# Kernel optimization log

Measured on AMD Instinct MI355X. Metric: run time of the kernel, lower is better.

Reference implementation:

```python
import jax, jax.numpy as jnp
import numpy as np

NH = 16      # num_attention_heads
NKV = 8      # num_key_value_heads
G = NH // NKV  # num_key_value_groups
D = 128      # head_dim = hidden_size // NH
ROPE_MAX = 2048


def _rope_tables(seq_len, dtype=jnp.float32):
    # matches RotaryEmbedding: inv_freq over even dims, freqs duplicated (concat), cos/sin cached
    inv_freq = 1.0 / (10000.0 ** (jnp.arange(0, D, 2, dtype=jnp.float32) / D))
    t = jnp.arange(ROPE_MAX, dtype=jnp.float32)[:, None]          # [max, 1]
    freqs = t * inv_freq[None, :]                                  # [max, D/2]
    freqs = jnp.concatenate((freqs, freqs), axis=-1)               # [max, D]
    cos = jnp.cos(freqs)[:seq_len].astype(dtype)                   # [S, D]
    sin = jnp.sin(freqs)[:seq_len].astype(dtype)
    # unsqueeze(0) then unsqueeze(2) -> [1, S, 1, D] broadcasting over batch and heads
    return cos[None, :, None, :], sin[None, :, None, :]


def _rotate_half(x):
    x1, x2 = jnp.split(x, 2, axis=-1)
    return jnp.concatenate((-x2, x1), axis=-1)


def setup_inputs() -> dict:
    key = jax.random.key(0)
    ks = jax.random.split(key, 5)
    B, S, H = 2, 2048, 2048
    scale = 1.0 / np.sqrt(H)
    return {
        "hidden_states": jax.random.normal(ks[0], (B, S, H), jnp.float32),
        "Wq": jax.random.normal(ks[1], (H, H), jnp.float32) * scale,
        "Wk": jax.random.normal(ks[2], (NKV * D, H), jnp.float32) * scale,
        "Wv": jax.random.normal(ks[3], (NKV * D, H), jnp.float32) * scale,
        "Wo": jax.random.normal(ks[4], (H, H), jnp.float32) * scale,
    }


def reference(hidden_states, Wq, Wk, Wv, Wo):
    B, S, H = hidden_states.shape
    # projections (nn.Linear: y = x @ W.T, no bias)
    q = (hidden_states @ Wq.T).reshape(B, S, NH, D)     # [B,S,NH,D]
    k = (hidden_states @ Wk.T).reshape(B, S, NKV, D)    # [B,S,NKV,D]
    v = (hidden_states @ Wv.T).reshape(B, S, NKV, D)

    cos, sin = _rope_tables(S, hidden_states.dtype)
    q = q * cos + _rotate_half(q) * sin
    k = k * cos + _rotate_half(k) * sin

    # GQA: query head h attends to kv head h // G (repeat_kv ordering: h = n*G + g)
    qg = q.reshape(B, S, NKV, G, D).transpose(0, 2, 3, 1, 4)   # [B,NKV,G,S,D]
    kt = k.transpose(0, 2, 1, 3)                                # [B,NKV,S,D]
    vt = v.transpose(0, 2, 1, 3)                                # [B,NKV,S,D]

    scores = jnp.einsum("bngqd,bnkd->bngqk", qg, kt) / np.sqrt(D)  # [B,NKV,G,S,S]
    causal = jnp.triu(jnp.ones((S, S), dtype=bool), k=1)
    neg = jnp.finfo(scores.dtype).min
    scores = jnp.where(causal[None, None, None], neg, scores)
    probs = jax.nn.softmax(scores.astype(jnp.float32), axis=-1).astype(q.dtype)

    out = jnp.einsum("bngqk,bnkd->bngqd", probs, vt)            # [B,NKV,G,S,D]
    out = out.transpose(0, 3, 1, 2, 4).reshape(B, S, H)         # [B,S,H]
    return out @ Wo.T
```

## Files before the change

kernel.cpp:

```cpp
#include <hip/hip_runtime.h>

typedef unsigned short u16;
typedef __attribute__((ext_vector_type(8))) short short8;
typedef __attribute__((ext_vector_type(4))) float f32x4;

__device__ __forceinline__ u16 f2bf(float f) {
  unsigned u = __float_as_uint(f);
  return (u16)((u + 0x7FFFu + ((u >> 16) & 1u)) >> 16);
}
__device__ __forceinline__ float bf2f(u16 h) {
  return __uint_as_float(((unsigned)h) << 16);
}

__device__ __forceinline__ void gload_lds16(const void* g, void* l) {
  __builtin_amdgcn_global_load_lds(
      (const __attribute__((address_space(1))) unsigned*)g,
      (__attribute__((address_space(3))) unsigned*)l, 16, 0, 0);
}

__global__ void cast_f32_bf16_k(const float4* __restrict__ in, u16* __restrict__ out, int n4) {
  int i = blockIdx.x * 256 + threadIdx.x;
  if (i >= n4) return;
  float4 v = in[i];
  union { u16 u[4]; uint2 d; } r;
  r.u[0] = f2bf(v.x); r.u[1] = f2bf(v.y); r.u[2] = f2bf(v.z); r.u[3] = f2bf(v.w);
  *reinterpret_cast<uint2*>(out + (size_t)i * 4) = r.d;
}

__global__ void rope_tables_k(float* __restrict__ cosT, float* __restrict__ sinT) {
  int idx = blockIdx.x * 256 + threadIdx.x;
  int i = idx & 63, s = idx >> 6;
  double inv = pow(10000.0, -(double)(2 * i) / 128.0);
  double f = (double)s * inv;
  cosT[idx] = (float)cos(f);
  sinT[idx] = (float)sin(f);
}

__global__ void rope_q_k(u16* __restrict__ x, const float* __restrict__ cosT,
                         const float* __restrict__ sinT) {
  int idx = blockIdx.x * 256 + threadIdx.x;
  int i = idx & 63;
  int hh = (idx >> 6) & 15;
  int row = idx >> 10;
  int s = row & 2047;
  size_t base = (size_t)row * 4096 + hh * 128;
  float x1 = bf2f(x[base + i]);
  float x2 = bf2f(x[base + i + 64]);
  float c = cosT[s * 64 + i], sn = sinT[s * 64 + i];
  x[base + i]      = f2bf(x1 * c - x2 * sn);
  x[base + i + 64] = f2bf(x2 * c + x1 * sn);
}

__global__ void rope_repack_k_k(const u16* __restrict__ qkv, u16* __restrict__ kt,
                                const float* __restrict__ cosT, const float* __restrict__ sinT) {
  int idx = blockIdx.x * 256 + threadIdx.x;
  int i = idx & 63;
  int kvh = (idx >> 6) & 7;
  int row = idx >> 9;
  int s = row & 2047, b = row >> 11;
  size_t src = (size_t)row * 4096 + 2048 + kvh * 128;
  float x1 = bf2f(qkv[src + i]);
  float x2 = bf2f(qkv[src + i + 64]);
  float c = cosT[s * 64 + i], sn = sinT[s * 64 + i];
  size_t dst = ((size_t)(b * 8 + kvh) * 2048 + s) * 128;
  kt[dst + i]      = f2bf(x1 * c - x2 * sn);
  kt[dst + i + 64] = f2bf(x2 * c + x1 * sn);
}

__global__ void transpose_v_k(const u16* __restrict__ qkv, u16* __restrict__ vt) {
  __shared__ u16 tile[128][129];
  int bn = blockIdx.y;
  int s0 = blockIdx.x * 128;
  int b = bn >> 3, n = bn & 7;
  for (int e = threadIdx.x; e < 128 * 128; e += 256) {
    int r = e >> 7, c = e & 127;
    tile[r][c] = qkv[(size_t)(b * 2048 + s0 + r) * 4096 + 3072 + n * 128 + c];
  }
  __syncthreads();
  for (int e = threadIdx.x; e < 128 * 128; e += 256) {
    int r = e >> 7, c = e & 127;
    vt[((size_t)bn * 128 + r) * 2048 + s0 + c] = tile[c][r];
  }
}

template<typename OutT, int BN>
__global__ __launch_bounds__(512, 1) void gemm256_k(
    const u16* __restrict__ A, const u16* __restrict__ Bm,
    OutT* __restrict__ C, int M, int N, int K)
{
  constexpr int BITER = (BN * 8) / 512;
  constexpr int NFR = BN / 64;
  __shared__ __align__(16) u16 As[2][256 * 64];
  __shared__ __align__(16) u16 Bs[2][BN * 64];
  const int tid = threadIdx.x;
  const int wave = tid >> 6, lane = tid & 63;
  const int wm = wave >> 2, wn = wave & 3;
  const int lrow = lane & 15, lgrp = lane >> 4;
  const int gx = (int)gridDim.x;
  const int nwg = gx * (int)gridDim.y;
  const int f = (int)(blockIdx.y * gridDim.x + blockIdx.x);
  const int sw = (f & 7) * (nwg >> 3) + (f >> 3);
  const int bx = sw % gx, by = sw / gx;
  const int row0 = by * 256, col0 = bx * BN;

  f32x4 acc[8][NFR];
  #pragma unroll
  for (int m = 0; m < 8; ++m)
    #pragma unroll
    for (int n = 0; n < NFR; ++n) acc[m][n] = (f32x4){0.f, 0.f, 0.f, 0.f};

  const int NT = K >> 6;

  auto stage = [&](int buf, int k0) {
    #pragma unroll
    for (int i = 0; i < 4; ++i) {
      int cid = i * 512 + tid;
      int row = cid >> 3, cp = cid & 7;
      int c = cp ^ (row & 7);
      gload_lds16(A + (size_t)(row0 + row) * K + k0 + c * 8,
                  &As[buf][(size_t)(i * 512 + wave * 64) * 8]);
    }
    #pragma unroll
    for (int i = 0; i < BITER; ++i) {
      int cid = i * 512 + tid;
      int row = cid >> 3, cp = cid & 7;
      int c = cp ^ (row & 7);
      gload_lds16(Bm + (size_t)(col0 + row) * K + k0 + c * 8,
                  &Bs[buf][(size_t)(i * 512 + wave * 64) * 8]);
    }
  };

  stage(0, 0);
  for (int t = 0; t < NT; ++t) {
    const int cur = t & 1;
    if (t + 1 < NT) {
      stage(cur ^ 1, (t + 1) << 6);
      if constexpr (BN == 256) asm volatile("s_waitcnt vmcnt(8)" ::: "memory");
      else                     asm volatile("s_waitcnt vmcnt(6)" ::: "memory");
    } else {
      asm volatile("s_waitcnt vmcnt(0)" ::: "memory");
    }
    __builtin_amdgcn_s_barrier();
    __builtin_amdgcn_sched_barrier(0);
    #pragma unroll
    for (int ks = 0; ks < 2; ++ks) {
      short8 af[8], bfr[NFR];
      #pragma unroll
      for (int m = 0; m < 8; ++m) {
        int row = wm * 128 + m * 16 + lrow;
        int cp = (ks * 4 + lgrp) ^ (row & 7);
        af[m] = *reinterpret_cast<const short8*>(&As[cur][row * 64 + cp * 8]);
      }
      #pragma unroll
      for (int n = 0; n < NFR; ++n) {
        int row = wn * (NFR * 16) + n * 16 + lrow;
        int cp = (ks * 4 + lgrp) ^ (row & 7);
        bfr[n] = *reinterpret_cast<const short8*>(&Bs[cur][row * 64 + cp * 8]);
      }
      #pragma unroll
      for (int m = 0; m < 8; ++m)
        #pragma unroll
        for (int n = 0; n < NFR; ++n)
          acc[m][n] = __builtin_amdgcn_mfma_f32_16x16x32_bf16(af[m], bfr[n], acc[m][n], 0, 0, 0);
    }
    __builtin_amdgcn_sched_barrier(0);
    __builtin_amdgcn_s_barrier();
  }

  #pragma unroll
  for (int m = 0; m < 8; ++m)
    #pragma unroll
    for (int n = 0; n < NFR; ++n)
      #pragma unroll
      for (int j = 0; j < 4; ++j) {
        int r = row0 + wm * 128 + m * 16 + lgrp * 4 + j;
        int col = col0 + wn * (NFR * 16) + n * 16 + lrow;
        float val = acc[m][n][j];
        if constexpr (sizeof(OutT) == 2) C[(size_t)r * N + col] = f2bf(val);
        else                             C[(size_t)r * N + col] = val;
      }
}

__global__ __launch_bounds__(256, 2) void flash_attn_k(
    const u16* __restrict__ qkv, const u16* __restrict__ kt,
    const u16* __restrict__ vt, u16* __restrict__ o)
{
  constexpr int S = 2048, NH = 16, NKV = 8, D = 128;
  const int wave = threadIdx.x >> 6, lane = threadIdx.x & 63;
  const int flat = blockIdx.x;
  const int pr = flat >> 5;
  const int bh = (flat & 7) * 4 + ((flat >> 3) & 3);
  const int b = bh >> 4, h = bh & 15;
  const int kvh = h >> 1;
  const int lrow = lane & 15, lgrp = lane >> 4;

  __shared__ __align__(16) u16 ks[2][64 * 128];
  __shared__ __align__(16) u16 vs[2][128 * 64];

  const float scl2 = 0.12754245006443634f;
  const u16* khead = kt + (size_t)(b * NKV + kvh) * S * D;
  const u16* vhead = vt + (size_t)(b * NKV + kvh) * D * S;

  auto stage = [&](int nxt, int kv0n) {
    #pragma unroll
    for (int i = 0; i < 4; ++i) {
      int c = i * 256 + wave * 64 + lane;
      int kr = c >> 4;
      int kc16 = (c & 15) ^ (kr & 7);
      gload_lds16(khead + (size_t)(kv0n + kr) * D + kc16 * 8,
                  &ks[nxt][(size_t)(i * 256 + wave * 64) * 8]);
      int vr = c >> 3;
      int vc = (c & 7) ^ (vr & 7);
      gload_lds16(vhead + (size_t)vr * S + kv0n + vc * 8,
                  &vs[nxt][(size_t)(i * 256 + wave * 64) * 8]);
    }
  };

  #pragma unroll
  for (int ph = 0; ph < 2; ++ph) {
    const int qt = ph ? pr : (31 - pr);
    const int q0 = qt * 64 + wave * 16;
    const int trips = qt + 1;

    short8 qf[4];
    const u16* qbase = qkv + (size_t)(b * S + q0 + lrow) * 4096 + h * 128;
    #pragma unroll
    for (int kc = 0; kc < 4; ++kc)
      qf[kc] = *reinterpret_cast<const short8*>(qbase + kc * 32 + lgrp * 8);

    f32x4 acc[8];
    #pragma unroll
    for (int n = 0; n < 8; ++n) acc[n] = (f32x4){0.f, 0.f, 0.f, 0.f};
    float l_part[4] = {0.f, 0.f, 0.f, 0.f};

    stage(0, 0);
    __syncthreads();

    for (int t = 0; t < trips; ++t) {
      const int cur = t & 1;
      const int kv0 = t * 64;
      f32x4 sc[4];
      #pragma unroll
      for (int nb = 0; nb < 4; ++nb) {
        sc[nb] = (f32x4){0.f, 0.f, 0.f, 0.f};
        const int r = nb * 16 + lrow;
        #pragma unroll
        for (int kc = 0; kc < 4; ++kc) {
          int ch = (kc * 4 + lgrp) ^ (r & 7);
          short8 kf = *reinterpret_cast<const short8*>(&ks[cur][r * 128 + ch * 8]);
          sc[nb] = __builtin_amdgcn_mfma_f32_16x16x32_bf16(qf[kc], kf, sc[nb], 0, 0, 0);
        }
      }
      __syncthreads();
      if (t + 1 < trips) stage(cur ^ 1, kv0 + 64);
      u16* pb = &ks[cur][wave * 1024];
      if (t < trips - 1) {
        #pragma unroll
        for (int nb = 0; nb < 4; ++nb)
          #pragma unroll
          for (int j = 0; j < 4; ++j) {
            int qr = lgrp * 4 + j;
            float p = exp2f(fminf(sc[nb][j] * scl2, 43.f));
            l_part[j] += p;
            pb[qr * 64 + ((nb * 16 + lrow) ^ ((qr & 7) << 3))] = f2bf(p);
          }
      } else {
        #pragma unroll
        for (int nb = 0; nb < 4; ++nb) {
          if (nb < wave) {
            #pragma unroll
            for (int j = 0; j < 4; ++j) {
              int qr = lgrp * 4 + j;
              float p = exp2f(fminf(sc[nb][j] * scl2, 43.f));
              l_part[j] += p;
              pb[qr * 64 + ((nb * 16 + lrow) ^ ((qr & 7) << 3))] = f2bf(p);
            }
          } else if (nb == wave) {
            #pragma unroll
            for (int j = 0; j < 4; ++j) {
              int qr = lgrp * 4 + j;
              float p = (lrow <= qr) ? exp2f(fminf(sc[nb][j] * scl2, 43.f)) : 0.f;
              l_part[j] += p;
              pb[qr * 64 + ((nb * 16 + lrow) ^ ((qr & 7) << 3))] = f2bf(p);
            }
          } else {
            #pragma unroll
            for (int j = 0; j < 4; ++j) {
              int qr = lgrp * 4 + j;
              pb[qr * 64 + ((nb * 16 + lrow) ^ ((qr & 7) << 3))] = 0;
            }
          }
        }
      }
      short8 pf[2];
      #pragma unroll
      for (int kc2 = 0; kc2 < 2; ++kc2) {
        int ch = (kc2 * 4 + lgrp) ^ (lrow & 7);
        pf[kc2] = *reinterpret_cast<const short8*>(&pb[lrow * 64 + ch * 8]);
      }
      #pragma unroll
      for (int n = 0; n < 8; ++n) {
        const int d = n * 16 + lrow;
        #pragma unroll
        for (int kc2 = 0; kc2 < 2; ++kc2) {
          int ch = (kc2 * 4 + lgrp) ^ (d & 7);
          short8 vf = *reinterpret_cast<const short8*>(&vs[cur][d * 64 + ch * 8]);
          acc[n] = __builtin_amdgcn_mfma_f32_16x16x32_bf16(pf[kc2], vf, acc[n], 0, 0, 0);
        }
      }
      __syncthreads();
    }

    float inv[4];
    #pragma unroll
    for (int j = 0; j < 4; ++j) {
      float s = l_part[j];
      #pragma unroll
      for (int off = 8; off; off >>= 1) s += __shfl_xor(s, off);
      inv[j] = 1.f / s;
    }
    u16* obase = o + (((size_t)(b * S + q0)) * NH + h) * D;
    #pragma unroll
    for (int n = 0; n < 8; ++n)
      #pragma unroll
      for (int j = 0; j < 4; ++j)
        obase[(size_t)(lgrp * 4 + j) * NH * D + n * 16 + lrow] = f2bf(acc[n][j] * inv[j]);
    __syncthreads();
  }
}

extern "C" void kernel_launch(void* const* d_in, const int* in_sizes, int n_in,
                              void* d_out, int out_size, void* d_ws, size_t ws_size,
                              hipStream_t stream) {
  const float* hs = (const float*)d_in[0];
  const float* Wq = (const float*)d_in[1];
  const float* Wk = (const float*)d_in[2];
  const float* Wv = (const float*)d_in[3];
  const float* Wo = (const float*)d_in[4];
  float* out = (float*)d_out;

  constexpr int B = 2, S = 2048, H = 2048, NH = 16, NKV = 8, D = 128;
  constexpr int M = B * S;
  constexpr int NQKV = 4096;

  char* w = (char*)d_ws;
  auto alloc = [&](size_t bytes) { char* p = w; w += (bytes + 255) & ~(size_t)255; return p; };
  u16* hs_bf   = (u16*)alloc((size_t)M * H * 2);
  u16* wqkv_bf = (u16*)alloc((size_t)NQKV * H * 2);
  u16* wo_bf   = (u16*)alloc((size_t)H * H * 2);
  u16* qkv     = (u16*)alloc((size_t)M * NQKV * 2);
  float* cosT  = (float*)alloc((size_t)S * 64 * 4);
  float* sinT  = (float*)alloc((size_t)S * 64 * 4);
  u16* attn = hs_bf;
  u16* vt   = wqkv_bf;
  u16* kt   = wqkv_bf + (size_t)B * NKV * D * S;

  cast_f32_bf16_k<<<(M * H / 4) / 256, 256, 0, stream>>>((const float4*)hs, hs_bf, M * H / 4);
  cast_f32_bf16_k<<<(H * H / 4) / 256, 256, 0, stream>>>((const float4*)Wq, wqkv_bf, H * H / 4);
  cast_f32_bf16_k<<<(NKV * D * H / 4) / 256, 256, 0, stream>>>((const float4*)Wk, wqkv_bf + (size_t)2048 * H, NKV * D * H / 4);
  cast_f32_bf16_k<<<(NKV * D * H / 4) / 256, 256, 0, stream>>>((const float4*)Wv, wqkv_bf + (size_t)3072 * H, NKV * D * H / 4);
  cast_f32_bf16_k<<<(H * H / 4) / 256, 256, 0, stream>>>((const float4*)Wo, wo_bf, H * H / 4);
  rope_tables_k<<<(S * 64) / 256, 256, 0, stream>>>(cosT, sinT);

  gemm256_k<u16, 256><<<dim3(NQKV / 256, M / 256), 512, 0, stream>>>(hs_bf, wqkv_bf, qkv, M, NQKV, H);

  rope_q_k<<<(M * 16 * 64) / 256, 256, 0, stream>>>(qkv, cosT, sinT);
  rope_repack_k_k<<<(M * 8 * 64) / 256, 256, 0, stream>>>(qkv, kt, cosT, sinT);
  transpose_v_k<<<dim3(S / 128, B * NKV), 256, 0, stream>>>(qkv, vt);

  flash_attn_k<<<512, 256, 0, stream>>>(qkv, kt, vt, attn);

  gemm256_k<float, 128><<<dim3(H / 128, M / 256), 512, 0, stream>>>(attn, wo_bf, out, M, H, H);
}
```

Baseline: 238.0 us.

## Add finer-grained pipelined 256x256 GEMM for QKV projection

Adds a new GEMM kernel that splits each 64-wide K tile into two 32-wide halves and interleaves the prefetch of the next tile's A/B halves between MFMA groups. It uses explicit vmcnt waits, barriers and setprio so global-to-LDS loads overlap matrix-core work. The QKV projection now uses this kernel. The trade-offs are more barriers per K tile and a hand-tuned wait schedule that must stay correct.

```diff
diff --git a/kernel.cpp b/kernel.cpp
--- a/kernel.cpp
+++ b/kernel.cpp
@@ -81,6 +81,146 @@
     int r = e >> 7, c = e & 127;
     vt[((size_t)bn * 128 + r) * 2048 + s0 + c] = tile[c][r];
   }
+}
+
+template<typename OutT>
+__global__ __launch_bounds__(512, 1) void gemm256p_k(
+    const u16* __restrict__ A, const u16* __restrict__ Bm,
+    OutT* __restrict__ C, int M, int N, int K)
+{
+  __shared__ __align__(16) u16 As[2][2][256 * 32];
+  __shared__ __align__(16) u16 Bs[2][2][256 * 32];
+  const int tid = threadIdx.x;
+  const int wave = tid >> 6, lane = tid & 63;
+  const int wm = wave >> 2, wn = wave & 3;
+  const int lrow = lane & 15, lgrp = lane >> 4;
+  const int gx = (int)gridDim.x;
+  const int nwg = gx * (int)gridDim.y;
+  const int f = (int)(blockIdx.y * gridDim.x + blockIdx.x);
+  const int sw = (f & 7) * (nwg >> 3) + (f >> 3);
+  const int bx = sw % gx, by = sw / gx;
+  const int row0 = by * 256, col0 = bx * 256;
+
+  f32x4 acc[8][4];
+  #pragma unroll
+  for (int m = 0; m < 8; ++m)
+    #pragma unroll
+    for (int n = 0; n < 4; ++n) acc[m][n] = (f32x4){0.f, 0.f, 0.f, 0.f};
+
+  const int NT = K >> 6;
+  const int psw = lgrp ^ (lrow & 3);
+
+  auto stageA = [&](int buf, int t, int ks) {
+    const int k0 = (t << 6) + ks * 32;
+    #pragma unroll
+    for (int i = 0; i < 2; ++i) {
+      int s = i * 512 + tid;
+      int row = s >> 2, p = s & 3;
+      int g = p ^ (row & 3);
+      gload_lds16(A + (size_t)(row0 + row) * K + k0 + g * 8,
+                  &As[buf][ks][(size_t)(i * 512 + wave * 64) * 8]);
+    }
+  };
+  auto stageB = [&](int buf, int t, int ks) {
+    const int k0 = (t << 6) + ks * 32;
+    #pragma unroll
+    for (int i = 0; i < 2; ++i) {
+      int s = i * 512 + tid;
+      int row = s >> 2, p = s & 3;
+      int g = p ^ (row & 3);
+      gload_lds16(Bm + (size_t)(col0 + row) * K + k0 + g * 8,
+                  &Bs[buf][ks][(size_t)(i * 512 + wave * 64) * 8]);
+    }
+  };
+
+  stageA(0, 0, 0); stageB(0, 0, 0); stageA(0, 0, 1); stageB(0, 0, 1);
+
+  for (int t = 0; t < NT; ++t) {
+    const int cur = t & 1, nxt = cur ^ 1;
+    const bool pf = (t + 1 < NT);
+    short8 af[4], bfr[4];
+
+    if (pf) { stageA(nxt, t + 1, 0); asm volatile("s_waitcnt vmcnt(6)" ::: "memory"); }
+    else    {                        asm volatile("s_waitcnt vmcnt(4)" ::: "memory"); }
+    __builtin_amdgcn_s_barrier();
+    __builtin_amdgcn_sched_barrier(0);
+    #pragma unroll
+    for (int m = 0; m < 4; ++m)
+      af[m] = *reinterpret_cast<const short8*>(&As[cur][0][(wm * 128 + m * 16 + lrow) * 32 + psw * 8]);
+    #pragma unroll
+    for (int n = 0; n < 4; ++n)
+      bfr[n] = *reinterpret_cast<const short8*>(&Bs[cur][0][(wn * 64 + n * 16 + lrow) * 32 + psw * 8]);
+    asm volatile("s_waitcnt lgkmcnt(0)" ::: "memory");
+    __builtin_amdgcn_sched_barrier(0);
+    __builtin_amdgcn_s_setprio(1);
+    #pragma unroll
+    for (int m = 0; m < 4; ++m)
+      #pragma unroll
+      for (int n = 0; n < 4; ++n)
+        acc[m][n] = __builtin_amdgcn_mfma_f32_16x16x32_bf16(af[m], bfr[n], acc[m][n], 0, 0, 0);
+    __builtin_amdgcn_s_setprio(0);
+
+    if (pf) stageB(nxt, t + 1, 0);
+    #pragma unroll
+    for (int m = 0; m < 4; ++m)
+      af[m] = *reinterpret_cast<const short8*>(&As[cur][0][(wm * 128 + (m + 4) * 16 + lrow) * 32 + psw * 8]);
+    asm volatile("s_waitcnt lgkmcnt(0)" ::: "memory");
+    __builtin_amdgcn_sched_barrier(0);
+    __builtin_amdgcn_s_setprio(1);
+    #pragma unroll
+    for (int m = 0; m < 4; ++m)
+      #pragma unroll
+      for (int n = 0; n < 4; ++n)
+        acc[m + 4][n] = __builtin_amdgcn_mfma_f32_16x16x32_bf16(af[m], bfr[n], acc[m + 4][n], 0, 0, 0);
+    __builtin_amdgcn_s_setprio(0);
+
+    if (pf) { stageA(nxt, t + 1, 1); asm volatile("s_waitcnt vmcnt(6)" ::: "memory"); }
+    else    {                        asm volatile("s_waitcnt vmcnt(0)" ::: "memory"); }
+    __builtin_amdgcn_s_barrier();
+    __builtin_amdgcn_sched_barrier(0);
+    #pragma unroll
+    for (int m = 0; m < 4; ++m)
+      af[m] = *reinterpret_cast<const short8*>(&As[cur][1][(wm * 128 + m * 16 + lrow) * 32 + psw * 8]);
+    #pragma unroll
+    for (int n = 0; n < 4; ++n)
+      bfr[n] = *reinterpret_cast<const short8*>(&Bs[cur][1][(wn * 64 + n * 16 + lrow) * 32 + psw * 8]);
+    asm volatile("s_waitcnt lgkmcnt(0)" ::: "memory");
+    __builtin_amdgcn_sched_barrier(0);
+    __builtin_amdgcn_s_setprio(1);
+    #pragma unroll
+    for (int m = 0; m < 4; ++m)
+      #pragma unroll
+      for (int n = 0; n < 4; ++n)
+        acc[m][n] = __builtin_amdgcn_mfma_f32_16x16x32_bf16(af[m], bfr[n], acc[m][n], 0, 0, 0);
+    __builtin_amdgcn_s_setprio(0);
+
+    if (pf) stageB(nxt, t + 1, 1);
+    #pragma unroll
+    for (int m = 0; m < 4; ++m)
+      af[m] = *reinterpret_cast<const short8*>(&As[cur][1][(wm * 128 + (m + 4) * 16 + lrow) * 32 + psw * 8]);
+    asm volatile("s_waitcnt lgkmcnt(0)" ::: "memory");
+    __builtin_amdgcn_sched_barrier(0);
+    __builtin_amdgcn_s_setprio(1);
+    #pragma unroll
+    for (int m = 0; m < 4; ++m)
+      #pragma unroll
+      for (int n = 0; n < 4; ++n)
+        acc[m + 4][n] = __builtin_amdgcn_mfma_f32_16x16x32_bf16(af[m], bfr[n], acc[m + 4][n], 0, 0, 0);
+    __builtin_amdgcn_s_setprio(0);
+  }
+
+  #pragma unroll
+  for (int m = 0; m < 8; ++m)
+    #pragma unroll
+    for (int n = 0; n < 4; ++n)
+      #pragma unroll
+      for (int j = 0; j < 4; ++j) {
+        int r = row0 + wm * 128 + m * 16 + lgrp * 4 + j;
+        int col = col0 + wn * 64 + n * 16 + lrow;
+        float val = acc[m][n][j];
+        if constexpr (sizeof(OutT) == 2) C[(size_t)r * N + col] = f2bf(val);
+        else                             C[(size_t)r * N + col] = val;
+      }
 }
 
 template<typename OutT, int BN>
@@ -362,7 +502,7 @@
   cast_f32_bf16_k<<<(H * H / 4) / 256, 256, 0, stream>>>((const float4*)Wo, wo_bf, H * H / 4);
   rope_tables_k<<<(S * 64) / 256, 256, 0, stream>>>(cosT, sinT);
 
-  gemm256_k<u16, 256><<<dim3(NQKV / 256, M / 256), 512, 0, stream>>>(hs_bf, wqkv_bf, qkv, M, NQKV, H);
+  gemm256p_k<u16><<<dim3(NQKV / 256, M / 256), 512, 0, stream>>>(hs_bf, wqkv_bf, qkv, M, NQKV, H);
 
   rope_q_k<<<(M * 16 * 64) / 256, 256, 0, stream>>>(qkv, cosT, sinT);
   rope_repack_k_k<<<(M * 8 * 64) / 256, 256, 0, stream>>>(qkv, kt, cosT, sinT);
```

Result: no change. 234.5 us (-1.5%).
